# Kernel optimization log

Hardware: AMD Instinct MI355X
Metric: run time of the kernel (lower is better)

Reference implementation:

```python
import jax, jax.numpy as jnp
import numpy as np

K_MASK = -2.3819763e+38
NUM_HEADS = 16
NUM_KV_HEADS = 8
FEATURES = 2048
HEAD_DIM = 128
WINDOW = 1024
SOFT_CAP = 50.0
B, T = 2, 2048


def apply_rope(inputs, positions, head_dim, max_wavelength=10000):
    # inputs: [B, T, N, H], positions: [B, T]
    fraction = 2 * jnp.arange(0, head_dim // 2) / head_dim
    timescale = max_wavelength ** fraction
    sinusoid_inp = positions[..., None] / timescale[None, None, :]  # [B,T,H/2]
    sinusoid_inp = sinusoid_inp[..., None, :]  # [B,T,1,H/2]
    sin = jnp.sin(sinusoid_inp)
    cos = jnp.cos(sinusoid_inp)
    first_half, second_half = jnp.split(inputs, 2, axis=-1)
    first_part = first_half * cos - second_half * sin
    second_part = second_half * cos + first_half * sin
    return jnp.concatenate([first_part, second_part], axis=-1).astype(inputs.dtype)


def setup_inputs() -> dict:
    key = jax.random.key(0)
    k1, k2, k3, k4 = jax.random.split(key, 4)
    std = 0.02
    x = jax.random.normal(k1, (B, T, FEATURES), dtype=jnp.float32)
    segment_pos = jnp.broadcast_to(jnp.arange(T, dtype=jnp.int32), (B, T))
    # causal prefill mask [B, T, T]
    attn_mask = jnp.broadcast_to(jnp.tril(jnp.ones((T, T), dtype=bool)), (B, T, T))
    wq = jax.random.normal(k2, (NUM_HEADS, FEATURES, HEAD_DIM), dtype=jnp.float32) * std
    wkv = jax.random.normal(k3, (2, NUM_KV_HEADS, FEATURES, HEAD_DIM), dtype=jnp.float32) * std
    wo = jax.random.normal(k4, (NUM_HEADS, HEAD_DIM, FEATURES), dtype=jnp.float32) * std
    return {"x": x, "segment_pos": segment_pos, "attn_mask": attn_mask,
            "wq": wq, "wkv": wkv, "wo": wo}


def reference(x, segment_pos, attn_mask, wq, wkv, wo):
    # Projections (GQA path: num_kv_heads != num_heads)
    q = jnp.einsum('BTD,NDH->BTNH', x, wq)              # [B,T,N,H]
    k = jnp.einsum('BSD,KDH->BSKH', x, wkv[0])          # [B,S,K,H]
    v = jnp.einsum('BSD,KDH->BSKH', x, wkv[1])          # [B,S,K,H]

    q = apply_rope(q, segment_pos, HEAD_DIM)
    q = q * HEAD_DIM ** (-0.5)
    k = apply_rope(k, segment_pos, HEAD_DIM)

    b, t, n, h = q.shape
    g = n // NUM_KV_HEADS
    qg = q.reshape(b, t, NUM_KV_HEADS, g, h)
    logits = jnp.einsum('BTKGH,BSKH->BTKGS', qg, k)
    s = logits.shape[-1]
    logits = logits.reshape(b, t, n, s)

    # soft cap
    logits = jnp.tanh(logits / SOFT_CAP) * SOFT_CAP

    # sliding-window mask combined with attn_mask
    cache_positions = jnp.arange(s)[None, None, :]
    sp = segment_pos[:, :, None]
    sliding_mask = (cache_positions >= sp - WINDOW + 1) & (cache_positions <= sp + WINDOW - 1)
    mask = sliding_mask & attn_mask  # [B,T,S]

    padded_logits = jnp.where(mask[:, :, None, :], logits, K_MASK)
    probs = jax.nn.softmax(padded_logits, axis=-1).astype(k.dtype)

    pg = probs.reshape(b, t, NUM_KV_HEADS, g, s)
    encoded = jnp.einsum('BTKGS,BSKH->BTKGH', pg, v).reshape(b, t, n, h)
    attn_output = jnp.einsum('BTNH,NHD->BTD', encoded, wo)
    return attn_output
```

## Files before the change

### kernel.cpp

```cpp
#include <hip/hip_runtime.h>

typedef unsigned short u16;
typedef unsigned int u32;
typedef __attribute__((ext_vector_type(8))) short bfx8;
typedef __attribute__((ext_vector_type(4))) float fx4;

static __device__ __forceinline__ float b2f(u16 u) {
    union { float f; u32 i; } c; c.i = ((u32)u) << 16; return c.f;
}
static __device__ __forceinline__ u16 f2b(float f) {
    union { float f; u32 i; } c; c.f = f;
    u32 r = c.i + 0x7FFFu + ((c.i >> 16) & 1u);
    return (u16)(r >> 16);
}
typedef const __attribute__((address_space(1))) unsigned int* gas1;
typedef __attribute__((address_space(3))) unsigned int* las3;
static __device__ __forceinline__ void gll16(const void* g, void* l) {
    __builtin_amdgcn_global_load_lds((gas1)g, (las3)l, 16, 0, 0);
}

__global__ __launch_bounds__(256) void k_prep1(const float* __restrict__ x, u16* __restrict__ xb,
                                               const float* __restrict__ wq, const float* __restrict__ wkv,
                                               u16* __restrict__ wb1) {
    __shared__ float t[128 * 33];
    int bid = blockIdx.x, tid = threadIdx.x;
    if (bid < 4096) {
        size_t i = ((size_t)bid * 256 + tid) * 8;
        float4 a = *(const float4*)(x + i);
        float4 b = *(const float4*)(x + i + 4);
        union { u16 e[8]; uint4 v; } o;
        o.e[0] = f2b(a.x); o.e[1] = f2b(a.y); o.e[2] = f2b(a.z); o.e[3] = f2b(a.w);
        o.e[4] = f2b(b.x); o.e[5] = f2b(b.y); o.e[6] = f2b(b.z); o.e[7] = f2b(b.w);
        *(uint4*)(xb + i) = o.v;
        return;
    }
    int idx = bid - 4096;
    int ci = idx & 31;
    int k0 = (idx >> 5) << 5;
    int c0 = ci << 7;
    const float* src;
    if (ci < 16)      src = wq  + (size_t)ci * 2048 * 128;
    else if (ci < 24) src = wkv + (size_t)(ci - 16) * 2048 * 128;
    else              src = wkv + (size_t)(8 + ci - 24) * 2048 * 128;
#pragma unroll
    for (int i = 0; i < 16; i++) {
        int id2 = i * 256 + tid;
        int kk = id2 >> 7, cc = id2 & 127;
        t[cc * 33 + kk] = src[(size_t)(k0 + kk) * 128 + cc];
    }
    __syncthreads();
#pragma unroll
    for (int i = 0; i < 16; i++) {
        int id2 = i * 256 + tid;
        int cc = id2 >> 5, kk = id2 & 31;
        wb1[(size_t)(c0 + cc) * 2048 + k0 + kk] = f2b(t[cc * 33 + kk]);
    }
}

template <int BM, int OUT_BF16>
__global__ __launch_bounds__(512, 2) void k_gemm8p(const u16* __restrict__ A, const u16* __restrict__ Bt,
                                                   void* __restrict__ C, int M, int N, int K) {
    constexpr int MF = BM / 32;
    constexpr int MH = MF / 2;
    constexpr int AF = BM / 8;
    constexpr int FR = AF + 32;
    constexpr int LPW = FR / 8;
    __shared__ u16 lds[2 * FR * 512];

    int tid = threadIdx.x, wave = tid >> 6, lane = tid & 63;
    int quad = lane >> 4, l16 = lane & 15;
    int wm = wave >> 2, wn = wave & 3;

    int nwg = gridDim.x * gridDim.y;
    int bid = blockIdx.y * gridDim.x + blockIdx.x;
    int swz = (bid & 7) * (nwg >> 3) + (bid >> 3);
    int bx = swz % gridDim.x, by = swz / gridDim.x;
    int r0 = by * BM, c0 = bx << 8;

    fx4 zero = {0.f, 0.f, 0.f, 0.f};
    fx4 acc[MF][4];
#pragma unroll
    for (int m = 0; m < MF; m++)
#pragma unroll
        for (int n = 0; n < 4; n++) acc[m][n] = zero;

    const u16* gsrc[LPW];
#pragma unroll
    for (int j = 0; j < LPW; j++) {
        int fw = wave * LPW + j;
        const u16* base;
        if (fw < AF) base = A + (size_t)(r0 + (fw >> 1) * 16 + l16) * K;
        else { int g = fw - AF; base = Bt + (size_t)(c0 + (g >> 1) * 16 + l16) * K; }
        gsrc[j] = base + (fw & 1) * 32 + quad * 8;
    }

    int NT = K >> 6;
#pragma unroll
    for (int j = 0; j < LPW; j++) gll16(gsrc[j], lds + wave * (LPW * 512) + j * 512);
    asm volatile("s_waitcnt vmcnt(0)" : : : "memory");
    __builtin_amdgcn_s_barrier();

    bfx8 ax[MH][2], bu[2][2], bv[2][2];

#define MFMA_PH(AH, NB, BV)                                                                               \
    __builtin_amdgcn_s_setprio(1);                                                                        \
    _Pragma("unroll") for (int kk = 0; kk < 2; kk++)                                                      \
    _Pragma("unroll") for (int m = 0; m < MH; m++)                                                        \
    _Pragma("unroll") for (int n = 0; n < 2; n++)                                                         \
        acc[(AH) * MH + m][(NB) * 2 + n] =                                                                \
            __builtin_amdgcn_mfma_f32_16x16x32_bf16(ax[m][kk], BV[n][kk], acc[(AH) * MH + m][(NB) * 2 + n], 0, 0, 0); \
    __builtin_amdgcn_s_setprio(0);

    for (int T = 0; T < NT; ++T) {
        const u16* buf = lds + (T & 1) * (FR * 512);
        if (T + 1 < NT) {
            u16* dst = lds + ((T + 1) & 1) * (FR * 512) + wave * (LPW * 512);
#pragma unroll
            for (int j = 0; j < LPW; j++) gll16(gsrc[j] + (size_t)(T + 1) * 64, dst + j * 512);
        }
#pragma unroll
        for (int m = 0; m < MH; m++)
#pragma unroll
            for (int kk = 0; kk < 2; kk++)
                ax[m][kk] = *(const bfx8*)(buf + (((wm * MF + m) << 1) + kk) * 512 + lane * 8);
#pragma unroll
        for (int n = 0; n < 2; n++)
#pragma unroll
            for (int kk = 0; kk < 2; kk++)
                bu[n][kk] = *(const bfx8*)(buf + (AF + (((wn << 2) + n) << 1) + kk) * 512 + lane * 8);
        __builtin_amdgcn_s_barrier();
        MFMA_PH(0, 0, bu)
        __builtin_amdgcn_s_barrier();
#pragma unroll
        for (int n = 0; n < 2; n++)
#pragma unroll
            for (int kk = 0; kk < 2; kk++)
                bv[n][kk] = *(const bfx8*)(buf + (AF + (((wn << 2) + 2 + n) << 1) + kk) * 512 + lane * 8);
        __builtin_amdgcn_s_barrier();
        MFMA_PH(0, 1, bv)
        __builtin_amdgcn_s_barrier();
#pragma unroll
        for (int m = 0; m < MH; m++)
#pragma unroll
            for (int kk = 0; kk < 2; kk++)
                ax[m][kk] = *(const bfx8*)(buf + (((wm * MF + MH + m) << 1) + kk) * 512 + lane * 8);
        __builtin_amdgcn_s_barrier();
        MFMA_PH(1, 0, bu)
        __builtin_amdgcn_s_barrier();
        MFMA_PH(1, 1, bv)
        asm volatile("s_waitcnt vmcnt(0)" : : : "memory");
        __builtin_amdgcn_s_barrier();
    }
#undef MFMA_PH
#pragma unroll
    for (int m = 0; m < MF; m++)
#pragma unroll
        for (int n = 0; n < 4; n++) {
            int col = c0 + wn * 64 + n * 16 + l16;
#pragma unroll
            for (int r = 0; r < 4; r++) {
                int row = r0 + wm * (BM / 2) + m * 16 + quad * 4 + r;
                float v = acc[m][n][r];
                if (OUT_BF16) ((u16*)C)[(size_t)row * N + col] = f2b(v);
                else          ((float*)C)[(size_t)row * N + col] = v;
            }
        }
}

__global__ __launch_bounds__(256) void k_mid(u16* __restrict__ qkv, u16* __restrict__ Kb,
                                             u16* __restrict__ Vt,
                                             const float* __restrict__ wo, u16* __restrict__ wb2) {
    __shared__ __align__(16) char smem[128 * 136 * 2];
    int bid = blockIdx.x, tid = threadIdx.x;
    if (bid < 4096) {
        float* sc = (float*)smem;
        int b = bid >> 11, t = bid & 2047;
        u16* row = qkv + (size_t)bid * 4096;
        float tf = (float)t;
        const float RS = 0.08838834764831845f;
        const float LT = 0.20762050593046f;
        if (tid < 64) {
            float ang = tf * exp2f(-LT * (float)tid);
            float s, c; sincosf(ang, &s, &c);
            sc[tid] = s; sc[tid + 64] = c;
        }
        __syncthreads();
#pragma unroll
        for (int i = 0; i < 4; i++) {
            int idx = tid + i * 256;
            int n = idx >> 6, hp = idx & 63;
            float x1 = b2f(row[n * 128 + hp]);
            float x2 = b2f(row[n * 128 + hp + 64]);
            float s = sc[hp], c = sc[hp + 64];
            row[n * 128 + hp]      = f2b((x1 * c - x2 * s) * RS);
            row[n * 128 + hp + 64] = f2b((x2 * c + x1 * s) * RS);
        }
#pragma unroll
        for (int i = 0; i < 2; i++) {
            int idx = tid + i * 256;
            int kh = idx >> 6, hp = idx & 63;
            float x1 = b2f(row[2048 + kh * 128 + hp]);
            float x2 = b2f(row[2048 + kh * 128 + hp + 64]);
            float s = sc[hp], c = sc[hp + 64];
            size_t o = ((size_t)(b * 8 + kh) * 2048 + t) * 128 + hp;
            Kb[o]      = f2b(x1 * c - x2 * s);
            Kb[o + 64] = f2b(x2 * c + x1 * s);
        }
        return;
    }
    if (bid < 4352) {
        u16* t = (u16*)smem;
        int idx = bid - 4096;
        int bk = idx >> 4;
        int t0 = (idx & 15) << 7;
        const u16* src = qkv + ((size_t)((bk >> 3) * 2048 + t0)) * 4096 + 3072 + (bk & 7) * 128;
        u16* dst = Vt + (size_t)bk * 128 * 2048 + t0;
#pragma unroll
        for (int it = 0; it < 8; it++) {
            int ch = tid + it * 256;
            int tt = ch >> 4, c8 = (ch & 15) << 3;
            *(uint4*)(t + tt * 136 + c8) = *(const uint4*)(src + (size_t)tt * 4096 + c8);
        }
        __syncthreads();
#pragma unroll
        for (int it = 0; it < 8; it++) {
            int ch = tid + it * 256;
            int h = ch >> 4, s8 = (ch & 15) << 3;
            union { uint4 v; u16 e[8]; } vv;
#pragma unroll
            for (int j = 0; j < 8; j++) vv.e[j] = t[(s8 + j) * 136 + h];
            *(uint4*)(dst + (size_t)h * 2048 + s8) = vv.v;
        }
        return;
    }
    float* t = (float*)smem;
    int idx = bid - 4352;
    int c0 = (idx & 15) << 7;
    int k0 = (idx >> 4) << 5;
#pragma unroll
    for (int i = 0; i < 16; i++) {
        int id2 = i * 256 + tid;
        int kk = id2 >> 7, cc = id2 & 127;
        t[cc * 33 + kk] = wo[(size_t)(k0 + kk) * 2048 + c0 + cc];
    }
    __syncthreads();
#pragma unroll
    for (int i = 0; i < 16; i++) {
        int id2 = i * 256 + tid;
        int cc = id2 >> 5, kk = id2 & 31;
        wb2[(size_t)(c0 + cc) * 2048 + k0 + kk] = f2b(t[cc * 33 + kk]);
    }
}

__global__ __launch_bounds__(512, 4) void k_attn(const u16* __restrict__ qkv, const u16* __restrict__ Kb,
                                                 const u16* __restrict__ Vt, u16* __restrict__ enc) {
    __shared__ u16 Ks[2][16 * 512];
    __shared__ u16 Vs[2][16 * 512];
    __shared__ u16 Pl[8 * 1024];
    int t0 = blockIdx.x << 6;
    int kh = blockIdx.y, b = blockIdx.z;
    int tid = threadIdx.x, wave = tid >> 6, lane = tid & 63;
    int quad = lane >> 4, l16 = lane & 15;
    int n = (kh << 1) + (wave >> 2);
    int tw = t0 + ((wave & 3) << 4);
    const u16* Qp = qkv + (size_t)b * 2048 * 4096 + n * 128;
    const u16* Kp = Kb + (size_t)(b * 8 + kh) * 2048 * 128;
    const u16* Vp = Vt + (size_t)(b * 8 + kh) * 128 * 2048;

    bfx8 aq[4];
#pragma unroll
    for (int kb = 0; kb < 4; kb++)
        aq[kb] = *(const bfx8*)(Qp + (size_t)(tw + l16) * 4096 + kb * 32 + quad * 8);

    const u16* kgp[2]; const u16* vgp[2];
#pragma unroll
    for (int q = 0; q < 2; q++) {
        int f = wave * 2 + q;
        kgp[q] = Kp + (size_t)((f >> 2) * 16 + l16) * 128 + (f & 3) * 32 + quad * 8;
        vgp[q] = Vp + (size_t)((f >> 1) * 16 + l16) * 2048 + (f & 1) * 32 + quad * 8;
    }
    u16* Pw = Pl + wave * 1024;

    fx4 zero = {0.f, 0.f, 0.f, 0.f};
    fx4 o_acc[8];
#pragma unroll
    for (int hb = 0; hb < 8; hb++) o_acc[hb] = zero;
    float lsum[4] = {0.f, 0.f, 0.f, 0.f};

    const float C1 = 0.057707801635559f;
    const float C2 = 144.269504088896f;

    int s_lo = t0 - 1023; if (s_lo < 0) s_lo = 0;
    int ts0 = s_lo >> 6, ts1 = t0 >> 6;

#pragma unroll
    for (int q = 0; q < 2; q++) {
        int f = wave * 2 + q;
        gll16(kgp[q] + (size_t)(ts0 << 6) * 128, Ks[0] + f * 512);
        gll16(vgp[q] + (ts0 << 6), Vs[0] + f * 512);
    }

    for (int ts = ts0; ts <= ts1; ts++) {
        int cur = (ts - ts0) & 1;
        int s0 = ts << 6;
        __builtin_amdgcn_s_barrier();
        if (ts < ts1) {
            int s1 = (ts + 1) << 6;
#pragma unroll
            for (int q = 0; q < 2; q++) {
                int f = wave * 2 + q;
                gll16(kgp[q] + (size_t)s1 * 128, Ks[cur ^ 1] + f * 512);
                gll16(vgp[q] + s1, Vs[cur ^ 1] + f * 512);
            }
            asm volatile("s_waitcnt vmcnt(4)" : : : "memory");
        } else {
            asm volatile("s_waitcnt vmcnt(0)" : : : "memory");
        }
        __builtin_amdgcn_s_barrier();

        if (s0 <= tw + 15 && s0 + 63 >= tw - 1023) {
            const u16* Kc = Ks[cur];
            const u16* Vc = Vs[cur];
            bool full = (s0 + 63 <= tw) && (s0 >= tw - 1008);
            if (full) {
#pragma unroll
                for (int nb = 0; nb < 4; nb++) {
                    fx4 sacc = zero;
                    __builtin_amdgcn_s_setprio(1);
#pragma unroll
                    for (int kb = 0; kb < 4; kb++) {
                        bfx8 bk = *(const bfx8*)(Kc + (nb * 4 + kb) * 512 + lane * 8);
                        sacc = __builtin_amdgcn_mfma_f32_16x16x32_bf16(aq[kb], bk, sacc, 0, 0, 0);
                    }
                    __builtin_amdgcn_s_setprio(0);
                    int base0 = ((nb >> 1) * 64 + ((nb & 1) * 2 + (l16 >> 3)) * 16 + quad * 4) * 8 + (l16 & 7);
#pragma unroll
                    for (int r = 0; r < 4; r++) {
                        float u = __builtin_amdgcn_exp2f(sacc[r] * C1);
                        float p = __builtin_amdgcn_exp2f(-C2 * __builtin_amdgcn_rcpf(u + 1.f));
                        lsum[r] += p;
                        Pw[base0 + r * 8] = f2b(p);
                    }
                }
            } else {
#pragma unroll
                for (int nb = 0; nb < 4; nb++) {
                    int sb = s0 + (nb << 4);
                    int base0 = ((nb >> 1) * 64 + ((nb & 1) * 2 + (l16 >> 3)) * 16 + quad * 4) * 8 + (l16 & 7);
                    if (sb <= tw + 15 && sb + 15 >= tw - 1023) {
                        fx4 sacc = zero;
#pragma unroll
                        for (int kb = 0; kb < 4; kb++) {
                            bfx8 bk = *(const bfx8*)(Kc + (nb * 4 + kb) * 512 + lane * 8);
                            sacc = __builtin_amdgcn_mfma_f32_16x16x32_bf16(aq[kb], bk, sacc, 0, 0, 0);
                        }
                        int sg = sb + l16;
#pragma unroll
                        for (int r = 0; r < 4; r++) {
                            int tg = tw + quad * 4 + r;
                            float u = __builtin_amdgcn_exp2f(sacc[r] * C1);
                            float p = __builtin_amdgcn_exp2f(-C2 * __builtin_amdgcn_rcpf(u + 1.f));
                            p = (sg <= tg && sg >= tg - 1023) ? p : 0.f;
                            lsum[r] += p;
                            Pw[base0 + r * 8] = f2b(p);
                        }
                    } else {
#pragma unroll
                        for (int r = 0; r < 4; r++) Pw[base0 + r * 8] = 0;
                    }
                }
            }
            asm volatile("s_waitcnt lgkmcnt(0)" : : : "memory");
            __builtin_amdgcn_sched_barrier(0);
            bfx8 pf[2];
#pragma unroll
            for (int kk = 0; kk < 2; kk++)
                pf[kk] = *(const bfx8*)(Pw + kk * 512 + lane * 8);
            __builtin_amdgcn_s_setprio(1);
#pragma unroll
            for (int hb = 0; hb < 8; hb++)
#pragma unroll
                for (int kk = 0; kk < 2; kk++) {
                    bfx8 vf = *(const bfx8*)(Vc + (hb * 2 + kk) * 512 + lane * 8);
                    o_acc[hb] = __builtin_amdgcn_mfma_f32_16x16x32_bf16(pf[kk], vf, o_acc[hb], 0, 0, 0);
                }
            __builtin_amdgcn_s_setprio(0);
        }
    }
#pragma unroll
    for (int r = 0; r < 4; r++) {
#pragma unroll
        for (int off = 1; off < 16; off <<= 1)
            lsum[r] += __shfl_xor(lsum[r], off);
        lsum[r] = 1.0f / lsum[r];
    }
#pragma unroll
    for (int hb = 0; hb < 8; hb++) {
        int h = hb * 16 + l16;
#pragma unroll
        for (int r = 0; r < 4; r++) {
            int tg = tw + quad * 4 + r;
            enc[((size_t)(b * 2048 + tg) * 16 + n) * 128 + h] = f2b(o_acc[hb][r] * lsum[r]);
        }
    }
}

extern "C" void kernel_launch(void* const* d_in, const int* in_sizes, int n_in,
                              void* d_out, int out_size, void* d_ws, size_t ws_size,
                              hipStream_t stream) {
    const float* x   = (const float*)d_in[0];
    const float* wq  = (const float*)d_in[3];
    const float* wkv = (const float*)d_in[4];
    const float* wo  = (const float*)d_in[5];
    char* ws = (char*)d_ws;
    const size_t MiB = 1024 * 1024;
    u16* xb  = (u16*)(ws);
    u16* wb1 = (u16*)(ws + 16 * MiB);
    u16* qkv = (u16*)(ws + 32 * MiB);
    u16* Kb  = (u16*)(ws);
    u16* wb2 = (u16*)(ws + 8 * MiB);
    u16* enc = (u16*)(ws + 16 * MiB);
    u16* Vt  = (u16*)d_out;

    k_prep1<<<6144, 256, 0, stream>>>(x, xb, wq, wkv, wb1);
    k_gemm8p<256, 1><<<dim3(16, 16), 512, 0, stream>>>(xb, wb1, qkv, 4096, 4096, 2048);
    k_mid<<<5376, 256, 0, stream>>>(qkv, Kb, Vt, wo, wb2);
    k_attn<<<dim3(32, 8, 2), 512, 0, stream>>>(qkv, Kb, Vt, enc);
    k_gemm8p<128, 0><<<dim3(8, 32), 512, 0, stream>>>(enc, wb2, d_out, 4096, 2048, 2048);
}
```

Baseline: 365.9 us.

## Split GEMM prefetch into phase-ordered chunks with partial vmcnt waits

Restructures the double-buffered GEMM main loop so that global-to-LDS loads for the next tile are issued in three groups, ordered to match the compute phases that consume them. Each phase then waits with a partial vmcnt instead of a full drain, so the loop no longer ends with a blocking wait and the last tile is peeled. The aim is finer-grained overlap of loads with MFMA work and fewer full stalls. The cost is a more intricate mapping of loads to LDS slots and reliance on correct counter arithmetic across waves.

```diff
diff --git a/kernel.cpp b/kernel.cpp
--- a/kernel.cpp
+++ b/kernel.cpp
@@ -58,13 +58,15 @@
 }
 
 template <int BM, int OUT_BF16>
-__global__ __launch_bounds__(512, 2) void k_gemm8p(const u16* __restrict__ A, const u16* __restrict__ Bt,
+__global__ __launch_bounds__(512, 2) void k_gemmdw(const u16* __restrict__ A, const u16* __restrict__ Bt,
                                                    void* __restrict__ C, int M, int N, int K) {
     constexpr int MF = BM / 32;
     constexpr int MH = MF / 2;
     constexpr int AF = BM / 8;
     constexpr int FR = AF + 32;
     constexpr int LPW = FR / 8;
+    constexpr int C0 = (4 * MH + 16) / 8;
+    constexpr int C2 = MH / 2;
     __shared__ u16 lds[2 * FR * 512];
 
     int tid = threadIdx.x, wave = tid >> 6, lane = tid & 63;
@@ -85,73 +87,89 @@
         for (int n = 0; n < 4; n++) acc[m][n] = zero;
 
     const u16* gsrc[LPW];
+    int lof[LPW];
 #pragma unroll
     for (int j = 0; j < LPW; j++) {
-        int fw = wave * LPW + j;
-        const u16* base;
-        if (fw < AF) base = A + (size_t)(r0 + (fw >> 1) * 16 + l16) * K;
-        else { int g = fw - AF; base = Bt + (size_t)(c0 + (g >> 1) * 16 + l16) * K; }
-        gsrc[j] = base + (fw & 1) * 32 + quad * 8;
+        int isA, fi;
+        if (j < C0) {
+            int idx = wave * C0 + j;
+            if (idx < 4 * MH) {
+                int g = idx / (2 * MH), r = idx % (2 * MH);
+                isA = 1; fi = ((g * MF + (r >> 1)) << 1) + (r & 1);
+            } else {
+                int t = idx - 4 * MH;
+                int cg = ((t >> 2) << 2) + ((t >> 1) & 1);
+                isA = 0; fi = (cg << 1) + (t & 1);
+            }
+        } else if (j < C0 + 2) {
+            int t = wave * 2 + (j - C0);
+            int cg = ((t >> 2) << 2) + 2 + ((t >> 1) & 1);
+            isA = 0; fi = (cg << 1) + (t & 1);
+        } else {
+            int idx = wave * C2 + (j - C0 - 2);
+            int g = idx / (2 * MH), r = idx % (2 * MH);
+            isA = 1; fi = ((g * MF + MH + (r >> 1)) << 1) + (r & 1);
+        }
+        gsrc[j] = (isA ? A + (size_t)(r0 + (fi >> 1) * 16 + l16) * K
+                       : Bt + (size_t)(c0 + (fi >> 1) * 16 + l16) * K) + (fi & 1) * 32 + quad * 8;
+        lof[j] = (isA ? fi : AF + fi) * 512;
     }
 
     int NT = K >> 6;
 #pragma unroll
-    for (int j = 0; j < LPW; j++) gll16(gsrc[j], lds + wave * (LPW * 512) + j * 512);
-    asm volatile("s_waitcnt vmcnt(0)" : : : "memory");
-    __builtin_amdgcn_s_barrier();
+    for (int j = 0; j < LPW; j++) gll16(gsrc[j], lds + lof[j]);
 
     bfx8 ax[MH][2], bu[2][2], bv[2][2];
-
-#define MFMA_PH(AH, NB, BV)                                                                               \
-    __builtin_amdgcn_s_setprio(1);                                                                        \
-    _Pragma("unroll") for (int kk = 0; kk < 2; kk++)                                                      \
-    _Pragma("unroll") for (int m = 0; m < MH; m++)                                                        \
-    _Pragma("unroll") for (int n = 0; n < 2; n++)                                                         \
-        acc[(AH) * MH + m][(NB) * 2 + n] =                                                                \
-            __builtin_amdgcn_mfma_f32_16x16x32_bf16(ax[m][kk], BV[n][kk], acc[(AH) * MH + m][(NB) * 2 + n], 0, 0, 0); \
+#define PH(vm) asm volatile("s_waitcnt vmcnt(%0)" : : "n"(vm) : "memory"); __builtin_amdgcn_s_barrier();
+#define RD_A(h) _Pragma("unroll") for (int m = 0; m < MH; m++) _Pragma("unroll") for (int kk = 0; kk < 2; kk++) \
+        ax[m][kk] = *(const bfx8*)(buf + (((wm * MF + (h) * MH + m) << 1) + kk) * 512 + lane * 8);
+#define RD_B(dst, pair) _Pragma("unroll") for (int n = 0; n < 2; n++) _Pragma("unroll") for (int kk = 0; kk < 2; kk++) \
+        dst[n][kk] = *(const bfx8*)(buf + (AF + (((wn << 2) + (pair) * 2 + n) << 1) + kk) * 512 + lane * 8);
+#define MM(h, pair, B) __builtin_amdgcn_s_setprio(1);                                                      \
+    _Pragma("unroll") for (int kk = 0; kk < 2; kk++) _Pragma("unroll") for (int m = 0; m < MH; m++)        \
+    _Pragma("unroll") for (int n = 0; n < 2; n++)                                                          \
+        acc[(h) * MH + m][(pair) * 2 + n] =                                                                \
+            __builtin_amdgcn_mfma_f32_16x16x32_bf16(ax[m][kk], B[n][kk], acc[(h) * MH + m][(pair) * 2 + n], 0, 0, 0); \
     __builtin_amdgcn_s_setprio(0);
 
-    for (int T = 0; T < NT; ++T) {
+    for (int T = 0; T < NT - 1; ++T) {
         const u16* buf = lds + (T & 1) * (FR * 512);
-        if (T + 1 < NT) {
-            u16* dst = lds + ((T + 1) & 1) * (FR * 512) + wave * (LPW * 512);
-#pragma unroll
-            for (int j = 0; j < LPW; j++) gll16(gsrc[j] + (size_t)(T + 1) * 64, dst + j * 512);
-        }
-#pragma unroll
-        for (int m = 0; m < MH; m++)
-#pragma unroll
-            for (int kk = 0; kk < 2; kk++)
-                ax[m][kk] = *(const bfx8*)(buf + (((wm * MF + m) << 1) + kk) * 512 + lane * 8);
-#pragma unroll
-        for (int n = 0; n < 2; n++)
-#pragma unroll
-            for (int kk = 0; kk < 2; kk++)
-                bu[n][kk] = *(const bfx8*)(buf + (AF + (((wn << 2) + n) << 1) + kk) * 512 + lane * 8);
-        __builtin_amdgcn_s_barrier();
-        MFMA_PH(0, 0, bu)
-        __builtin_amdgcn_s_barrier();
-#pragma unroll
-        for (int n = 0; n < 2; n++)
-#pragma unroll
-            for (int kk = 0; kk < 2; kk++)
-                bv[n][kk] = *(const bfx8*)(buf + (AF + (((wn << 2) + 2 + n) << 1) + kk) * 512 + lane * 8);
-        __builtin_amdgcn_s_barrier();
-        MFMA_PH(0, 1, bv)
-        __builtin_amdgcn_s_barrier();
-#pragma unroll
-        for (int m = 0; m < MH; m++)
-#pragma unroll
-            for (int kk = 0; kk < 2; kk++)
-                ax[m][kk] = *(const bfx8*)(buf + (((wm * MF + MH + m) << 1) + kk) * 512 + lane * 8);
-        __builtin_amdgcn_s_barrier();
-        MFMA_PH(1, 0, bu)
-        __builtin_amdgcn_s_barrier();
-        MFMA_PH(1, 1, bv)
-        asm volatile("s_waitcnt vmcnt(0)" : : : "memory");
-        __builtin_amdgcn_s_barrier();
-    }
-#undef MFMA_PH
+        u16* nb = lds + ((T + 1) & 1) * (FR * 512);
+        size_t go = (size_t)(T + 1) * 64;
+#pragma unroll
+        for (int j = 0; j < C0; j++) gll16(gsrc[j] + go, nb + lof[j]);
+        PH(LPW)
+        RD_A(0) RD_B(bu, 0)
+        MM(0, 0, bu)
+#pragma unroll
+        for (int j = C0; j < C0 + 2; j++) gll16(gsrc[j] + go, nb + lof[j]);
+        PH(LPW)
+        RD_B(bv, 1)
+        MM(0, 1, bv)
+#pragma unroll
+        for (int j = C0 + 2; j < LPW; j++) gll16(gsrc[j] + go, nb + lof[j]);
+        PH(LPW)
+        RD_A(1)
+        MM(1, 0, bu)
+        MM(1, 1, bv)
+    }
+    {
+        const u16* buf = lds + ((NT - 1) & 1) * (FR * 512);
+        PH(LPW - C0)
+        RD_A(0) RD_B(bu, 0)
+        MM(0, 0, bu)
+        PH(C2)
+        RD_B(bv, 1)
+        MM(0, 1, bv)
+        PH(0)
+        RD_A(1)
+        MM(1, 0, bu)
+        MM(1, 1, bv)
+    }
+#undef PH
+#undef RD_A
+#undef RD_B
+#undef MM
 #pragma unroll
     for (int m = 0; m < MF; m++)
 #pragma unroll
@@ -423,8 +441,8 @@
     u16* Vt  = (u16*)d_out;
 
     k_prep1<<<6144, 256, 0, stream>>>(x, xb, wq, wkv, wb1);
-    k_gemm8p<256, 1><<<dim3(16, 16), 512, 0, stream>>>(xb, wb1, qkv, 4096, 4096, 2048);
+    k_gemmdw<256, 1><<<dim3(16, 16), 512, 0, stream>>>(xb, wb1, qkv, 4096, 4096, 2048);
     k_mid<<<5376, 256, 0, stream>>>(qkv, Kb, Vt, wo, wb2);
     k_attn<<<dim3(32, 8, 2), 512, 0, stream>>>(qkv, Kb, Vt, enc);
-    k_gemm8p<128, 0><<<dim3(8, 32), 512, 0, stream>>>(enc, wb2, d_out, 4096, 2048, 2048);
-}
+    k_gemmdw<128, 0><<<dim3(8, 32), 512, 0, stream>>>(enc, wb2, d_out, 4096, 2048, 2048);
+}
```

New measurement: 345.3 us. 5.6% less time.
